# Performance work log

Measured on AMD Instinct MI355X. Metric: run time of the kernel, lower is better.

## Reference

```python
import jax, jax.numpy as jnp
import numpy as np

EMBED = 768
HEADS = 12
HID = EMBED * HEADS  # 9216; head_dim == embed_dim in this module
EPS = 1e-5


def _layernorm(x, g, b):
    mu = jnp.mean(x, axis=-1, keepdims=True)
    var = jnp.mean(jnp.square(x - mu), axis=-1, keepdims=True)
    return (x - mu) * jax.lax.rsqrt(var + EPS) * g + b


def setup_inputs() -> dict:
    key = jax.random.key(0)
    ks = jax.random.split(key, 16)
    B, S = 4, 1024
    s_in = 1.0 / np.sqrt(EMBED)
    s_hid = 1.0 / np.sqrt(HID)
    return {
        "x": jax.random.normal(ks[0], (B, S, EMBED), jnp.float32),
        "ln1_g": jnp.ones((EMBED,), jnp.float32),
        "ln1_b": jnp.zeros((EMBED,), jnp.float32),
        "wq": jax.random.normal(ks[1], (EMBED, HID), jnp.float32) * s_in,
        "bq": jnp.zeros((HID,), jnp.float32),
        "wk": jax.random.normal(ks[2], (EMBED, HID), jnp.float32) * s_in,
        "bk": jnp.zeros((HID,), jnp.float32),
        "wv": jax.random.normal(ks[3], (EMBED, HID), jnp.float32) * s_in,
        "bv": jnp.zeros((HID,), jnp.float32),
        "wo": jax.random.normal(ks[4], (HID, EMBED), jnp.float32) * s_hid,
        "bo": jnp.zeros((EMBED,), jnp.float32),
        "ln2_g": jnp.ones((EMBED,), jnp.float32),
        "ln2_b": jnp.zeros((EMBED,), jnp.float32),
        "w1": jax.random.normal(ks[5], (EMBED, EMBED), jnp.float32) * s_in,
        "b1": jnp.zeros((EMBED,), jnp.float32),
        "w2": jax.random.normal(ks[6], (EMBED, EMBED), jnp.float32) * s_in,
        "b2": jnp.zeros((EMBED,), jnp.float32),
    }


def reference(x, ln1_g, ln1_b, wq, bq, wk, bk, wv, bv, wo, bo,
              ln2_g, ln2_b, w1, b1, w2, b2):
    B, S, D = x.shape
    H = HEADS
    nx = _layernorm(x, ln1_g, ln1_b)
    # QKV projections: each head gets a FULL embed_dim-wide slice (head_dim == D)
    q = (nx @ wq + bq).reshape(B, S, H, D)
    k = (nx @ wk + bk).reshape(B, S, H, D)
    v = (nx @ wv + bv).reshape(B, S, H, D)
    scores = jnp.einsum("bqhd,bkhd->bhqk", q, k) / jnp.sqrt(jnp.float32(D))
    # Original applies softmax over dim=1 of per-head [B,q,k] scores -> the QUERY axis
    attn = jax.nn.softmax(scores, axis=-2)
    ctx = jnp.einsum("bhqk,bkhd->bqhd", attn, v).reshape(B, S, H * D)
    x_att = ctx @ wo + bo
    x = x + x_att
    h = _layernorm(x, ln2_g, ln2_b)
    h = jax.nn.gelu(h @ w1 + b1, approximate=False)
    h = h @ w2 + b2
    return x + h
```

## Files before the change

kernel.cpp:

```cpp
#include <hip/hip_runtime.h>
#include <math.h>

#define D_EMB 768
#define HEADS 12
#define HID   9216
#define BATCH 4
#define SEQ   1024
#define M_ROWS 4096

typedef __attribute__((ext_vector_type(8))) short bf16x8;
typedef __attribute__((ext_vector_type(4))) float f32x4;

__device__ __forceinline__ float b2f(unsigned short u) {
    return __uint_as_float(((unsigned)u) << 16);
}
__device__ __forceinline__ unsigned short f2b(float f) {
    unsigned u = __float_as_uint(f);
    u += 0x7fffu + ((u >> 16) & 1u);
    return (unsigned short)(u >> 16);
}

__device__ __forceinline__ void async_copy16(const void* g, void* l) {
    __builtin_amdgcn_global_load_lds(
        (const __attribute__((address_space(1))) void*)g,
        (__attribute__((address_space(3))) void*)l, 16, 0, 0);
}

enum { EPI_BF16 = 0, EPI_SCALE_BF16 = 1, EPI_BIAS_BF16 = 2,
       EPI_BIAS_GELU_BF16 = 3, EPI_BIAS_RES_F32 = 4, EPI_F32_PART = 5 };

template<int EPI, int SWAP = 0, int XS = 0>
__global__ __launch_bounds__(256)
void gemm_bt(const unsigned short* __restrict__ A,
             const unsigned short* __restrict__ B,
             void* __restrict__ Cv,
             const float* __restrict__ bias,
             const float* __restrict__ resid,
             float scale, int K, int ksplit,
             int lda, int ldb, int ldc, int nh, int nbm, int nbn,
             long sAb, long sAh, long sBb, long sBh, long sCb, long sCh)
{
    __shared__ unsigned short As[2][128 * 32];
    __shared__ unsigned short Bs[2][128 * 32];

    int bm, bn, bz;
    if constexpr (XS) {
        const int lid = blockIdx.x;
        const int nb = nbm * nbn;
        const int xcd = lid & 7, j = lid >> 3;
        bz = xcd * ((4 * nh) >> 3) + j / nb;
        const int pos = j % nb;
        bm = pos / nbn;
        bn = pos % nbn;
    } else {
        bm = SWAP ? blockIdx.x : blockIdx.y;
        bn = SWAP ? blockIdx.y : blockIdx.x;
        bz = blockIdx.z;
    }

    int Kloop = K;
    const unsigned short* Ab;
    const unsigned short* Bb;
    long coff;
    if constexpr (EPI == EPI_F32_PART) {
        Ab = A + (long)bz * ksplit;
        Bb = B + (long)bz * ksplit;
        coff = (long)bz * sCb;
        Kloop = ksplit;
    } else {
        const int b = bz / nh, h = bz - b * nh;
        Ab = A + (long)b * sAb + (long)h * sAh;
        Bb = B + (long)b * sBb + (long)h * sBh;
        coff = (long)b * sCb + (long)h * sCh;
    }

    const int tid = threadIdx.x;
    const int c0 = tid, c1 = tid + 256;

    const unsigned short* Ap0 = Ab + (long)(bm * 128 + (c0 >> 2)) * lda + (c0 & 3) * 8;
    const unsigned short* Ap1 = Ab + (long)(bm * 128 + (c1 >> 2)) * lda + (c1 & 3) * 8;
    const unsigned short* Bp0 = Bb + (long)(bn * 128 + (c0 >> 2)) * ldb + (c0 & 3) * 8;
    const unsigned short* Bp1 = Bb + (long)(bn * 128 + (c1 >> 2)) * ldb + (c1 & 3) * 8;

    const int lane = tid & 63;
    const int wid = tid >> 6;
    const int wm = wid >> 1, wn = wid & 1;
    const int r = lane & 15, ks = lane >> 4;

    f32x4 acc[4][4] = {};

    async_copy16(Ap0, &As[0][c0 * 8]);
    async_copy16(Ap1, &As[0][c1 * 8]);
    async_copy16(Bp0, &Bs[0][c0 * 8]);
    async_copy16(Bp1, &Bs[0][c1 * 8]);
    Ap0 += 32; Ap1 += 32; Bp0 += 32; Bp1 += 32;
    __syncthreads();

    int cur = 0;
    for (int kt = 0; kt < Kloop; kt += 32) {
        if (kt + 32 < Kloop) {
            const int nxt = cur ^ 1;
            async_copy16(Ap0, &As[nxt][c0 * 8]);
            async_copy16(Ap1, &As[nxt][c1 * 8]);
            async_copy16(Bp0, &Bs[nxt][c0 * 8]);
            async_copy16(Bp1, &Bs[nxt][c1 * 8]);
            Ap0 += 32; Ap1 += 32; Bp0 += 32; Bp1 += 32;
        }

        bf16x8 af[4], bfr[4];
        #pragma unroll
        for (int m = 0; m < 4; m++)
            af[m] = *(const bf16x8*)&As[cur][(wm * 64 + m * 16 + r) * 32 + ks * 8];
        #pragma unroll
        for (int n = 0; n < 4; n++)
            bfr[n] = *(const bf16x8*)&Bs[cur][(wn * 64 + n * 16 + r) * 32 + ks * 8];

        #pragma unroll
        for (int m = 0; m < 4; m++)
            #pragma unroll
            for (int n = 0; n < 4; n++)
                acc[m][n] = __builtin_amdgcn_mfma_f32_16x16x32_bf16(
                    af[m], bfr[n], acc[m][n], 0, 0, 0);

        __syncthreads();
        cur ^= 1;
    }

    #pragma unroll
    for (int m = 0; m < 4; m++) {
        const int row0 = bm * 128 + wm * 64 + m * 16 + ks * 4;
        #pragma unroll
        for (int n = 0; n < 4; n++) {
            const int col = bn * 128 + wn * 64 + n * 16 + r;
            #pragma unroll
            for (int j = 0; j < 4; j++) {
                const int row = row0 + j;
                float v = acc[m][n][j];
                if constexpr (EPI == EPI_SCALE_BF16) v *= scale;
                if constexpr (EPI == EPI_BIAS_BF16 || EPI == EPI_BIAS_GELU_BF16 ||
                              EPI == EPI_BIAS_RES_F32) v += bias[col];
                if constexpr (EPI == EPI_BIAS_GELU_BF16)
                    v = 0.5f * v * (1.0f + erff(v * 0.70710678118654752f));
                if constexpr (EPI == EPI_BIAS_RES_F32) {
                    float* C = (float*)Cv;
                    C[coff + (long)row * ldc + col] = v + resid[(long)row * ldc + col];
                } else if constexpr (EPI == EPI_F32_PART) {
                    float* C = (float*)Cv;
                    C[coff + (long)row * ldc + col] = v;
                } else {
                    unsigned short* C = (unsigned short*)Cv;
                    C[coff + (long)row * ldc + col] = f2b(v);
                }
            }
        }
    }
}

__global__ __launch_bounds__(256)
void reduce_part(const f32x4* __restrict__ p, f32x4* __restrict__ x2,
                 int n4, int nsp)
{
    const int i = blockIdx.x * 256 + threadIdx.x;
    f32x4 a = x2[i];
    for (int s = 0; s < nsp; s++) {
        const f32x4 v = p[(long)s * n4 + i];
        a[0] += v[0]; a[1] += v[1]; a[2] += v[2]; a[3] += v[3];
    }
    x2[i] = a;
}

__global__ __launch_bounds__(256)
void transpose_w(const float* __restrict__ in, unsigned short* __restrict__ out,
                 int R, int C, int col0)
{
    __shared__ float t[32][33];
    const int c0 = blockIdx.x * 32, r0 = blockIdx.y * 32;
    const int tx = threadIdx.x & 31, ty = threadIdx.x >> 5;
    #pragma unroll
    for (int i = 0; i < 4; i++)
        t[ty + i * 8][tx] = in[(long)(r0 + ty + i * 8) * C + col0 + c0 + tx];
    __syncthreads();
    #pragma unroll
    for (int i = 0; i < 4; i++)
        out[(long)(c0 + ty + i * 8) * R + r0 + tx] = f2b(t[tx][ty + i * 8]);
}

__global__ __launch_bounds__(256)
void transpose_v(const unsigned short* __restrict__ v, unsigned short* __restrict__ vt,
                 int ng)
{
    __shared__ unsigned short t[32][34];
    const int bz = blockIdx.z;
    const int b = bz / ng, hl = bz - b * ng;
    const int d0 = blockIdx.x * 32, s0 = blockIdx.y * 32;
    const int tx = threadIdx.x & 31, ty = threadIdx.x >> 5;
    const int ld = ng * D_EMB;
    const unsigned short* vin = v + (long)b * SEQ * ld + (long)hl * D_EMB;
    #pragma unroll
    for (int i = 0; i < 4; i++)
        t[ty + i * 8][tx] = vin[(long)(s0 + ty + i * 8) * ld + d0 + tx];
    __syncthreads();
    unsigned short* vo = vt + (long)bz * D_EMB * SEQ;
    #pragma unroll
    for (int i = 0; i < 4; i++)
        vo[(long)(d0 + ty + i * 8) * SEQ + s0 + tx] = t[tx][ty + i * 8];
}

__global__ __launch_bounds__(256)
void ln_kernel(const float* __restrict__ x, const float* __restrict__ g,
               const float* __restrict__ bb, unsigned short* __restrict__ out)
{
    const int row = blockIdx.x;
    const float* xr = x + (long)row * D_EMB;
    const int t = threadIdx.x;
    float v0 = xr[t], v1 = xr[t + 256], v2 = xr[t + 512];
    float s = v0 + v1 + v2;
    float ss = v0 * v0 + v1 * v1 + v2 * v2;
    #pragma unroll
    for (int o = 32; o > 0; o >>= 1) {
        s += __shfl_down(s, o);
        ss += __shfl_down(ss, o);
    }
    __shared__ float red[8];
    __shared__ float mu_s, rs_s;
    const int wid = t >> 6;
    if ((t & 63) == 0) { red[wid] = s; red[4 + wid] = ss; }
    __syncthreads();
    if (t == 0) {
        float a = red[0] + red[1] + red[2] + red[3];
        float q = red[4] + red[5] + red[6] + red[7];
        float mu = a * (1.0f / D_EMB);
        float var = q * (1.0f / D_EMB) - mu * mu;
        mu_s = mu;
        rs_s = rsqrtf(var + 1e-5f);
    }
    __syncthreads();
    const float mu = mu_s, rs = rs_s;
    unsigned short* orow = out + (long)row * D_EMB;
    orow[t]       = f2b((v0 - mu) * rs * g[t]       + bb[t]);
    orow[t + 256] = f2b((v1 - mu) * rs * g[t + 256] + bb[t + 256]);
    orow[t + 512] = f2b((v2 - mu) * rs * g[t + 512] + bb[t + 512]);
}

__global__ __launch_bounds__(256)
void x2_init(const float* __restrict__ x, const float* __restrict__ bo,
             float* __restrict__ x2)
{
    const int row = blockIdx.x;
    const float* xr = x + (long)row * D_EMB;
    float* o = x2 + (long)row * D_EMB;
    const int t = threadIdx.x;
    o[t]       = xr[t]       + bo[t];
    o[t + 256] = xr[t + 256] + bo[t + 256];
    o[t + 512] = xr[t + 512] + bo[t + 512];
}

__global__ __launch_bounds__(256)
void col_softmax(unsigned short* __restrict__ s)
{
    const long base = (long)blockIdx.y * ((long)SEQ * SEQ);
    const int t63 = threadIdx.x & 63;
    const int part = threadIdx.x >> 6;
    const int col = blockIdx.x * 64 + t63;
    unsigned short* p = s + base + col;
    const int q0 = part * 256;
    float m = -1e30f, sum = 0.0f;
    for (int q = q0; q < q0 + 256; q++) {
        float v = b2f(p[(long)q * SEQ]);
        float mn = fmaxf(m, v);
        sum = sum * __expf(m - mn) + __expf(v - mn);
        m = mn;
    }
    __shared__ float lm[4][64], ls[4][64];
    lm[part][t63] = m;
    ls[part][t63] = sum;
    __syncthreads();
    const float M = fmaxf(fmaxf(lm[0][t63], lm[1][t63]),
                          fmaxf(lm[2][t63], lm[3][t63]));
    const float S = ls[0][t63] * __expf(lm[0][t63] - M)
                  + ls[1][t63] * __expf(lm[1][t63] - M)
                  + ls[2][t63] * __expf(lm[2][t63] - M)
                  + ls[3][t63] * __expf(lm[3][t63] - M);
    const float inv = 1.0f / S;
    for (int q = q0; q < q0 + 256; q++) {
        float v = b2f(p[(long)q * SEQ]);
        p[(long)q * SEQ] = f2b(__expf(v - M) * inv);
    }
}

extern "C" void kernel_launch(void* const* d_in, const int* in_sizes, int n_in,
                              void* d_out, int out_size, void* d_ws, size_t ws_size,
                              hipStream_t stream)
{
    const float* x    = (const float*)d_in[0];
    const float* ln1g = (const float*)d_in[1];
    const float* ln1b = (const float*)d_in[2];
    const float* wq   = (const float*)d_in[3];
    const float* bq   = (const float*)d_in[4];
    const float* wk   = (const float*)d_in[5];
    const float* bk   = (const float*)d_in[6];
    const float* wv   = (const float*)d_in[7];
    const float* bv   = (const float*)d_in[8];
    const float* wo   = (const float*)d_in[9];
    const float* bo   = (const float*)d_in[10];
    const float* ln2g = (const float*)d_in[11];
    const float* ln2b = (const float*)d_in[12];
    const float* w1   = (const float*)d_in[13];
    const float* b1   = (const float*)d_in[14];
    const float* w2   = (const float*)d_in[15];
    const float* b2   = (const float*)d_in[16];
    float* out = (float*)d_out;

    auto a256 = [](size_t b) { return (b + 255) & ~(size_t)255; };

    auto plan_bytes = [&](int g) -> size_t {
        size_t o = 0;
        o += a256((size_t)D_EMB * D_EMB * 2);
        o += a256((size_t)D_EMB * D_EMB * 2);
        o += a256((size_t)M_ROWS * D_EMB * 2);
        o += a256((size_t)M_ROWS * D_EMB * 2);
        o += a256((size_t)M_ROWS * D_EMB * 4);
        o += a256((size_t)3 * g * D_EMB * D_EMB * 2);
        o += 3 * a256((size_t)M_ROWS * (size_t)g * D_EMB * 2);
        size_t vr = (size_t)M_ROWS * (size_t)g * D_EMB * 2;
        size_t sc = (size_t)BATCH * g * SEQ * SEQ * 2;
        o += a256(vr > sc ? vr : sc);
        return o;
    };
    const int cand[6] = {12, 6, 4, 3, 2, 1};
    int G = 1;
    for (int i = 0; i < 6; i++) {
        if (plan_bytes(cand[i]) <= ws_size) { G = cand[i]; break; }
    }
    const int NG = G * D_EMB;

    char* ws = (char*)d_ws;
    size_t off = 0;
    auto alloc = [&](size_t bytes) {
        void* p = ws + off;
        off += a256(bytes);
        return p;
    };
    unsigned short* w1T = (unsigned short*)alloc((size_t)D_EMB * D_EMB * 2);
    unsigned short* w2T = (unsigned short*)alloc((size_t)D_EMB * D_EMB * 2);
    unsigned short* nx  = (unsigned short*)alloc((size_t)M_ROWS * D_EMB * 2);
    unsigned short* h1  = (unsigned short*)alloc((size_t)M_ROWS * D_EMB * 2);
    float* x2           = (float*)alloc((size_t)M_ROWS * D_EMB * 4);
    unsigned short* wsl = (unsigned short*)alloc((size_t)3 * NG * D_EMB * 2);
    unsigned short* qg  = (unsigned short*)alloc((size_t)M_ROWS * NG * 2);
    unsigned short* kg  = (unsigned short*)alloc((size_t)M_ROWS * NG * 2);
    unsigned short* vtg = (unsigned short*)alloc((size_t)M_ROWS * NG * 2);
    {
        size_t vr = (size_t)M_ROWS * NG * 2;
        size_t sc = (size_t)BATCH * G * SEQ * SEQ * 2;
        (void)alloc(vr > sc ? vr : sc);
    }
    unsigned short* vr  = vtg + (size_t)M_ROWS * NG;
    unsigned short* scg = vr;
    unsigned short* ctx = qg;

    const size_t part_one = (size_t)M_ROWS * D_EMB * 4;
    const size_t avail = 2 * (size_t)M_ROWS * NG * 2;
    int nsp = 4;
    while (nsp > 1 && (size_t)nsp * part_one > avail) nsp >>= 1;
    while (nsp > 1 && (NG / nsp) % 32 != 0) nsp >>= 1;
    float* part = (float*)kg;

    const dim3 blk(256);
    const float scl = 0.03608439182435161f;
    const int nbh = BATCH * G;
    const bool xs_ok = (nbh % 8) == 0;

    ln_kernel<<<dim3(M_ROWS), blk, 0, stream>>>(x, ln1g, ln1b, nx);
    x2_init<<<dim3(M_ROWS), blk, 0, stream>>>(x, bo, x2);
    transpose_w<<<dim3(D_EMB / 32, D_EMB / 32), blk, 0, stream>>>(w1, w1T, D_EMB, D_EMB, 0);
    transpose_w<<<dim3(D_EMB / 32, D_EMB / 32), blk, 0, stream>>>(w2, w2T, D_EMB, D_EMB, 0);

    const int ngrp = HEADS / G;
    for (int g = 0; g < ngrp; g++) {
        const int h0 = g * G;
        unsigned short* wslQ = wsl;
        unsigned short* wslK = wsl + (size_t)NG * D_EMB;
        unsigned short* wslV = wsl + (size_t)2 * NG * D_EMB;
        transpose_w<<<dim3(NG / 32, D_EMB / 32), blk, 0, stream>>>(wq, wslQ, D_EMB, HID, h0 * D_EMB);
        transpose_w<<<dim3(NG / 32, D_EMB / 32), blk, 0, stream>>>(wk, wslK, D_EMB, HID, h0 * D_EMB);
        transpose_w<<<dim3(NG / 32, D_EMB / 32), blk, 0, stream>>>(wv, wslV, D_EMB, HID, h0 * D_EMB);

        gemm_bt<EPI_BIAS_BF16, 1><<<dim3(M_ROWS / 128, NG / 128, 1), blk, 0, stream>>>(
            nx, wslQ, qg, bq + h0 * D_EMB, nullptr,
            1.0f, D_EMB, 0, D_EMB, D_EMB, NG, 1, 0, 0, 0, 0, 0, 0, 0, 0);
        gemm_bt<EPI_BIAS_BF16, 1><<<dim3(M_ROWS / 128, NG / 128, 1), blk, 0, stream>>>(
            nx, wslK, kg, bk + h0 * D_EMB, nullptr,
            1.0f, D_EMB, 0, D_EMB, D_EMB, NG, 1, 0, 0, 0, 0, 0, 0, 0, 0);
        gemm_bt<EPI_BIAS_BF16, 1><<<dim3(M_ROWS / 128, NG / 128, 1), blk, 0, stream>>>(
            nx, wslV, vr, bv + h0 * D_EMB, nullptr,
            1.0f, D_EMB, 0, D_EMB, D_EMB, NG, 1, 0, 0, 0, 0, 0, 0, 0, 0);
        transpose_v<<<dim3(D_EMB / 32, SEQ / 32, BATCH * G), blk, 0, stream>>>(vr, vtg, G);

        if (xs_ok) {
            gemm_bt<EPI_SCALE_BF16, 0, 1><<<dim3(nbh * 64, 1, 1), blk, 0, stream>>>(
                qg, kg, scg, nullptr, nullptr,
                scl, D_EMB, 0, NG, NG, SEQ, G, 8, 8,
                (long)SEQ * NG, D_EMB, (long)SEQ * NG, D_EMB,
                (long)G * SEQ * SEQ, (long)SEQ * SEQ);
        } else {
            gemm_bt<EPI_SCALE_BF16><<<dim3(SEQ / 128, SEQ / 128, nbh), blk, 0, stream>>>(
                qg, kg, scg, nullptr, nullptr,
                scl, D_EMB, 0, NG, NG, SEQ, G, 0, 0,
                (long)SEQ * NG, D_EMB, (long)SEQ * NG, D_EMB,
                (long)G * SEQ * SEQ, (long)SEQ * SEQ);
        }

        col_softmax<<<dim3(SEQ / 64, nbh), blk, 0, stream>>>(scg);

        if (xs_ok) {
            gemm_bt<EPI_BF16, 0, 1><<<dim3(nbh * 48, 1, 1), blk, 0, stream>>>(
                scg, vtg, ctx, nullptr, nullptr,
                1.0f, SEQ, 0, SEQ, SEQ, NG, G, 8, 6,
                (long)G * SEQ * SEQ, (long)SEQ * SEQ,
                (long)G * D_EMB * SEQ, (long)D_EMB * SEQ,
                (long)SEQ * NG, (long)D_EMB);
        } else {
            gemm_bt<EPI_BF16><<<dim3(D_EMB / 128, SEQ / 128, nbh), blk, 0, stream>>>(
                scg, vtg, ctx, nullptr, nullptr,
                1.0f, SEQ, 0, SEQ, SEQ, NG, G, 0, 0,
                (long)G * SEQ * SEQ, (long)SEQ * SEQ,
                (long)G * D_EMB * SEQ, (long)D_EMB * SEQ,
                (long)SEQ * NG, (long)D_EMB);
        }

        transpose_w<<<dim3(D_EMB / 32, NG / 32), blk, 0, stream>>>(
            wo + (long)h0 * D_EMB * D_EMB, wsl, NG, D_EMB, 0);
        gemm_bt<EPI_F32_PART><<<dim3(D_EMB / 128, M_ROWS / 128, nsp), blk, 0, stream>>>(
            ctx, wsl, part, nullptr, nullptr,
            1.0f, NG, NG / nsp, NG, NG, D_EMB, 1, 0, 0,
            0, 0, 0, 0, (long)M_ROWS * D_EMB, 0);
        reduce_part<<<dim3(M_ROWS * D_EMB / 4 / 256), blk, 0, stream>>>(
            (const f32x4*)part, (f32x4*)x2, M_ROWS * D_EMB / 4, nsp);
    }

    ln_kernel<<<dim3(M_ROWS), blk, 0, stream>>>(x2, ln2g, ln2b, nx);

    gemm_bt<EPI_BIAS_GELU_BF16><<<dim3(D_EMB / 128, M_ROWS / 128, 1), blk, 0, stream>>>(
        nx, w1T, h1, b1, nullptr,
        1.0f, D_EMB, 0, D_EMB, D_EMB, D_EMB, 1, 0, 0, 0, 0, 0, 0, 0, 0);

    gemm_bt<EPI_BIAS_RES_F32><<<dim3(D_EMB / 128, M_ROWS / 128, 1), blk, 0, stream>>>(
        h1, w2T, out, b2, x2,
        1.0f, D_EMB, 0, D_EMB, D_EMB, D_EMB, 1, 0, 0, 0, 0, 0, 0, 0, 0);
}
```

Baseline: 847.3 us.

## Fuse Q/K/V projections into one 256x256-tile 8-wave MFMA GEMM

Replaces three separate 128x128 GEMM launches for the Q, K and V projections with a single kernel. It uses 256x256 tiles, 512 threads, 128KB of dynamic LDS and a finer-grained quarter-step prefetch pipeline, and routes each output tile to the Q, K or V buffer by column range. The goal is fewer launches, more operand reuse per tile and better MFMA utilisation. The cost is much higher LDS and register pressure, which lowers occupancy. The kernel also relies on the concatenated wsl layout and assumes NG is a multiple of 256 so that no tile straddles two outputs.

```diff
diff --git a/kernel.cpp b/kernel.cpp
--- a/kernel.cpp
+++ b/kernel.cpp
@@ -28,6 +28,134 @@
 
 enum { EPI_BF16 = 0, EPI_SCALE_BF16 = 1, EPI_BIAS_BF16 = 2,
        EPI_BIAS_GELU_BF16 = 3, EPI_BIAS_RES_F32 = 4, EPI_F32_PART = 5 };
+
+__global__ __launch_bounds__(512, 2)
+void gemm_qkv8(const unsigned short* __restrict__ A,
+               const unsigned short* __restrict__ B,
+               unsigned short* __restrict__ Cq,
+               unsigned short* __restrict__ Ck,
+               unsigned short* __restrict__ Cv,
+               const float* __restrict__ bq,
+               const float* __restrict__ bk,
+               const float* __restrict__ bv,
+               int K, int lda, int ldb, int ldc)
+{
+    extern __shared__ unsigned short lds[];
+    const int tid = threadIdx.x;
+    const int lane = tid & 63;
+    const int wid = tid >> 6;
+    const int wm = wid >> 2;
+    const int wn = wid & 3;
+    const int bm = blockIdx.x, bn = blockIdx.y;
+
+    const int r = lane & 15, ks = lane >> 4;
+    const int swz_src = (((lane & 7) ^ (lane >> 3)) * 8);
+    const int l8 = lane * 8;
+
+    const unsigned short* Ag = A + (long)(bm * 256) * lda;
+    const unsigned short* Bg = B + (long)(bn * 256) * ldb;
+
+    auto ldsA = [&](int buf) -> unsigned short* { return lds + buf * 32768; };
+    auto ldsB = [&](int buf) -> unsigned short* { return lds + buf * 32768 + 16384; };
+
+    auto stageA = [&](int buf, int reg, int kt) {
+        unsigned short* base = ldsA(buf);
+        #pragma unroll
+        for (int i = 0; i < 2; i++) {
+            const int idx = i * 64 + wid * 8;
+            const int row = (reg ? 64 : 0) + (idx & 63) + ((idx >> 6) << 7);
+            const unsigned short* src = Ag + (long)(row + (lane >> 3)) * lda
+                                        + kt * 64 + swz_src;
+            async_copy16(src, base + row * 64 + l8);
+        }
+    };
+    auto stageB = [&](int buf, int reg, int kt) {
+        unsigned short* base = ldsB(buf);
+        #pragma unroll
+        for (int i = 0; i < 2; i++) {
+            const int idx = i * 64 + wid * 8;
+            const int row = ((idx >> 5) << 6) + (reg ? 32 : 0) + (idx & 31);
+            const unsigned short* src = Bg + (long)(row + (lane >> 3)) * ldb
+                                        + kt * 64 + swz_src;
+            async_copy16(src, base + row * 64 + l8);
+        }
+    };
+    auto readA = [&](int buf, int m, int s) {
+        const int row = wm * 128 + m * 16 + r;
+        const int cg = (ks + s * 4) ^ (lane & 7);
+        return *(const bf16x8*)&ldsA(buf)[row * 64 + cg * 8];
+    };
+    auto readB = [&](int buf, int n, int s) {
+        const int row = wn * 64 + n * 16 + r;
+        const int cg = (ks + s * 4) ^ (lane & 7);
+        return *(const bf16x8*)&ldsB(buf)[row * 64 + cg * 8];
+    };
+
+    f32x4 acc[8][4] = {};
+    const int nt = K >> 6;
+
+    stageA(0, 0, 0); stageB(0, 0, 0); stageB(0, 1, 0); stageA(0, 1, 0);
+    if (nt > 1) { stageA(1, 0, 1); stageB(1, 0, 1); }
+    asm volatile("s_waitcnt vmcnt(4)" ::: "memory");
+    __builtin_amdgcn_s_barrier();
+
+    for (int t = 0; t < nt; t++) {
+        const int buf = t & 1, obuf = buf ^ 1;
+        #pragma unroll
+        for (int q = 0; q < 4; q++) {
+            const int mq = q >> 1, nh = q & 1;
+            if (q > 0 || t > 0) {
+                asm volatile("s_waitcnt vmcnt(8)" ::: "memory");
+                __builtin_amdgcn_s_barrier();
+            }
+            if (q == 0)      { if (t + 1 < nt) stageB(obuf, 1, t + 1); }
+            else if (q == 1) { if (t + 1 < nt) stageA(obuf, 1, t + 1); }
+            else if (q == 2) { if (t + 2 < nt) stageA(buf, 0, t + 2); }
+            else             { if (t + 2 < nt) stageB(buf, 0, t + 2); }
+
+            bf16x8 af[4][2], bfv[2][2];
+            #pragma unroll
+            for (int mi = 0; mi < 4; mi++)
+                #pragma unroll
+                for (int s = 0; s < 2; s++)
+                    af[mi][s] = readA(buf, mq * 4 + mi, s);
+            #pragma unroll
+            for (int ni = 0; ni < 2; ni++)
+                #pragma unroll
+                for (int s = 0; s < 2; s++)
+                    bfv[ni][s] = readB(buf, nh * 2 + ni, s);
+
+            __builtin_amdgcn_s_setprio(1);
+            #pragma unroll
+            for (int mi = 0; mi < 4; mi++)
+                #pragma unroll
+                for (int ni = 0; ni < 2; ni++)
+                    #pragma unroll
+                    for (int s = 0; s < 2; s++)
+                        acc[mq * 4 + mi][nh * 2 + ni] =
+                            __builtin_amdgcn_mfma_f32_16x16x32_bf16(
+                                af[mi][s], bfv[ni][s],
+                                acc[mq * 4 + mi][nh * 2 + ni], 0, 0, 0);
+            __builtin_amdgcn_s_setprio(0);
+        }
+    }
+
+    const int third = (bn * 256) / ldc;
+    unsigned short* C = (third == 0) ? Cq : (third == 1) ? Ck : Cv;
+    const float* bs = (third == 0) ? bq : (third == 1) ? bk : bv;
+    #pragma unroll
+    for (int m = 0; m < 8; m++) {
+        const int row0 = bm * 256 + wm * 128 + m * 16 + ks * 4;
+        #pragma unroll
+        for (int n = 0; n < 4; n++) {
+            const int cl = bn * 256 + wn * 64 + n * 16 + r - third * ldc;
+            const float bsv = bs[cl];
+            #pragma unroll
+            for (int j = 0; j < 4; j++)
+                C[(long)(row0 + j) * ldc + cl] = f2b(acc[m][n][j] + bsv);
+        }
+    }
+}
 
 template<int EPI, int SWAP = 0, int XS = 0>
 __global__ __launch_bounds__(256)
@@ -371,6 +499,13 @@
     const int nbh = BATCH * G;
     const bool xs_ok = (nbh % 8) == 0;
 
+    static bool attr_set = false;
+    if (!attr_set) {
+        hipFuncSetAttribute((const void*)gemm_qkv8,
+                            hipFuncAttributeMaxDynamicSharedMemorySize, 131072);
+        attr_set = true;
+    }
+
     ln_kernel<<<dim3(M_ROWS), blk, 0, stream>>>(x, ln1g, ln1b, nx);
     x2_init<<<dim3(M_ROWS), blk, 0, stream>>>(x, bo, x2);
     transpose_w<<<dim3(D_EMB / 32, D_EMB / 32), blk, 0, stream>>>(w1, w1T, D_EMB, D_EMB, 0);
@@ -386,16 +521,11 @@
         transpose_w<<<dim3(NG / 32, D_EMB / 32), blk, 0, stream>>>(wk, wslK, D_EMB, HID, h0 * D_EMB);
         transpose_w<<<dim3(NG / 32, D_EMB / 32), blk, 0, stream>>>(wv, wslV, D_EMB, HID, h0 * D_EMB);
 
-        gemm_bt<EPI_BIAS_BF16, 1><<<dim3(M_ROWS / 128, NG / 128, 1), blk, 0, stream>>>(
-            nx, wslQ, qg, bq + h0 * D_EMB, nullptr,
-            1.0f, D_EMB, 0, D_EMB, D_EMB, NG, 1, 0, 0, 0, 0, 0, 0, 0, 0);
-        gemm_bt<EPI_BIAS_BF16, 1><<<dim3(M_ROWS / 128, NG / 128, 1), blk, 0, stream>>>(
-            nx, wslK, kg, bk + h0 * D_EMB, nullptr,
-            1.0f, D_EMB, 0, D_EMB, D_EMB, NG, 1, 0, 0, 0, 0, 0, 0, 0, 0);
-        gemm_bt<EPI_BIAS_BF16, 1><<<dim3(M_ROWS / 128, NG / 128, 1), blk, 0, stream>>>(
-            nx, wslV, vr, bv + h0 * D_EMB, nullptr,
-            1.0f, D_EMB, 0, D_EMB, D_EMB, NG, 1, 0, 0, 0, 0, 0, 0, 0, 0);
-        transpose_v<<<dim3(D_EMB / 32, SEQ / 32, BATCH * G), blk, 0, stream>>>(vr, vtg, G);
+        gemm_qkv8<<<dim3(M_ROWS / 256, 3 * NG / 256, 1), dim3(512), 131072, stream>>>(
+            nx, wsl, qg, kg, vr,
+            bq + h0 * D_EMB, bk + h0 * D_EMB, bv + h0 * D_EMB,
+            D_EMB, D_EMB, D_EMB, NG);
+        transpose_v<<<dim3(D_EMB / 32, SEQ / 32, nbh), blk, 0, stream>>>(vr, vtg, G);
 
         if (xs_ok) {
             gemm_bt<EPI_SCALE_BF16, 0, 1><<<dim3(nbh * 64, 1, 1), blk, 0, stream>>>(
```

Result: faster. 801.1 us (-5.5%).
